# Optimization experiments

Hardware: AMD Instinct MI355X
Metric: run time of the kernel (lower is better)

The kernel has to match this reference:

```python
import jax, jax.numpy as jnp
import numpy as np
from jax import lax

B, S, DM = 4, 4096, 1024
H, P, R = 16, 32, 8
D = DM // H  # head_dim = 64
K_SEL = 4


def setup_inputs() -> dict:
    key = jax.random.key(0)
    ks = jax.random.split(key, 6)
    x = jax.random.normal(ks[0], (B, S, DM), dtype=jnp.float32)
    K_state = jax.random.normal(ks[1], (H, P, R, D), dtype=jnp.float32) / np.sqrt(D)
    V_state = jax.random.normal(ks[2], (H, P, R, D), dtype=jnp.float32) / np.sqrt(D)
    W_router = jax.random.normal(ks[3], (H, D, P), dtype=jnp.float32) / np.sqrt(D)
    W_out = jax.random.normal(ks[4], (DM, DM), dtype=jnp.float32) / np.sqrt(DM)
    b_out = jnp.zeros((DM,), dtype=jnp.float32)
    return {"x": x, "K_state": K_state, "V_state": V_state,
            "W_router": W_router, "W_out": W_out, "b_out": b_out, "k": K_SEL}


def reference(x, K_state, V_state, W_router, W_out, b_out, k):
    b, s, dm = x.shape
    h, p, r, d = K_state.shape
    xh = x.reshape(b, s, h, d)  # per-head token features

    # Router: top-k partition selection per token per head.
    logits = jnp.einsum('bshd,hdp->bshp', xh, W_router)
    topv = lax.top_k(logits, k)[0]            # [b,s,h,k]
    thresh = topv[..., -1:]                   # k-th largest logit
    neg_inf = jnp.array(-jnp.inf, dtype=logits.dtype)
    gates = jax.nn.softmax(jnp.where(logits >= thresh, logits, neg_inf), axis=-1)  # [b,s,h,p], zero off top-k

    # Attention over state rows within each partition (masked-dense == sparse gather math).
    scale = jnp.asarray(1.0 / np.sqrt(d), dtype=x.dtype)
    scores = jnp.einsum('bshd,hprd->bshpr', xh, K_state) * scale
    attn = jax.nn.softmax(scores, axis=-1)    # softmax over rows r within a partition

    # Gate-weighted combine of per-partition attention outputs, fused to avoid [b,s,h,p,d].
    w = attn * gates[..., None]               # [b,s,h,p,r]
    heads = jnp.einsum('bshpr,hprd->bshd', w, V_state)

    out = heads.reshape(b, s, dm) @ W_out + b_out
    return out
```

## Files before the change

kernel.cpp:

```cpp
#include <hip/hip_runtime.h>
#include <hip/hip_bf16.h>

#define BB 4
#define SS 4096
#define DM 1024
#define HH 16
#define PP 32
#define RR 8
#define DD 64
#define NTOK (BB*SS)
#define MM NTOK
#define NN DM
#define KK DM

typedef __attribute__((ext_vector_type(8))) short short8;
typedef __attribute__((ext_vector_type(4))) float floatx4;

static __device__ inline short f2bf(float f) {
    union { __hip_bfloat16 b; short s; } u; u.b = __float2bfloat16(f); return u.s;
}
static __device__ inline short8 pack8(float4 lo, float4 hi) {
    short8 r;
    r[0] = f2bf(lo.x); r[1] = f2bf(lo.y); r[2] = f2bf(lo.z); r[3] = f2bf(lo.w);
    r[4] = f2bf(hi.x); r[5] = f2bf(hi.y); r[6] = f2bf(hi.z); r[7] = f2bf(hi.w);
    return r;
}

static __device__ inline unsigned bfr(float f) {
    unsigned u = __float_as_uint(f);
    return u + 0x7fffu + ((u >> 16) & 1u);
}
static __device__ inline int pk2(float a, float b) {
    return __builtin_amdgcn_perm(bfr(b), bfr(a), 0x07060302);
}
static __device__ inline short8 pk8(float4 lo, float4 hi) {
    union { short8 s; int i[4]; } r;
    r.i[0] = pk2(lo.x, lo.y); r.i[1] = pk2(lo.z, lo.w);
    r.i[2] = pk2(hi.x, hi.y); r.i[3] = pk2(hi.z, hi.w);
    return r.s;
}

__global__ __launch_bounds__(256) void pre_fused(const float* __restrict__ x,
                                                 const float* __restrict__ Wr,
                                                 const int* __restrict__ kp,
                                                 const float* __restrict__ Wo,
                                                 const float* __restrict__ Kst,
                                                 const float* __restrict__ Vst,
                                                 float* __restrict__ gates_g,
                                                 __hip_bfloat16* __restrict__ wsw,
                                                 __hip_bfloat16* __restrict__ kfrag,
                                                 __hip_bfloat16* __restrict__ vfrag,
                                                 __hip_bfloat16* __restrict__ xbf) {
    const int bx = blockIdx.x;

    if (bx >= 4096) {
        if (bx < 4608) {
            int tid = (bx - 4096) * 256 + threadIdx.x;
            int l = tid & 63;
            int kblk = (tid >> 6) & 31;
            int ntile = tid >> 11;
            int col = ntile * 16 + (l & 15);
            int krow = kblk * 32 + (l >> 4) * 8;
#pragma unroll
            for (int j = 0; j < 8; ++j)
                wsw[(size_t)tid * 8 + j] = __float2bfloat16(Wo[(size_t)(krow + j) * NN + col]);
        } else if (bx < 4864) {
            int tid = (bx - 4608) * 256 + threadIdx.x;
            int arr = tid >> 15;
            int idx = tid & 32767;
            int h = idx >> 11, blk = (idx >> 6) & 31, fl = idx & 63;
            int fm = fl & 15, fk = fl >> 4;
            short8 val;
            short* dst;
            if (arr == 0) {
                int mt = blk >> 1, kb = blk & 1;
                int pr = mt * 16 + fm, d0 = kb * 32 + fk * 8;
                const float* src = Kst + ((size_t)h * 256 + pr) * 64 + d0;
                float4 lo = *(const float4*)src, hi = *(const float4*)(src + 4);
                val = pack8(lo, hi);
                dst = (short*)kfrag + (size_t)idx * 8;
            } else {
                int mt = blk >> 3, kb = blk & 7;
                int d = mt * 16 + fm, pr0 = kb * 32 + fk * 8;
                const float* src = Vst + ((size_t)h * 256 + pr0) * 64 + d;
#pragma unroll
                for (int j = 0; j < 8; ++j) val[j] = f2bf(src[j * 64]);
                dst = (short*)vfrag + (size_t)idx * 8;
            }
            *(short8*)dst = val;
        } else {
            int xid = bx - 4864;
            int tile = xid & 255, h = xid >> 8;
            int lane = threadIdx.x & 63, w = threadIdx.x >> 6;
            int l15 = lane & 15, l4 = lane >> 4;
            const float* srcb = x + (size_t)(tile * 64 + w * 16 + l15) * DM + h * 64 + l4 * 8;
            short* dstb = (short*)xbf + ((size_t)((h * 256 + tile) * 8 + w * 2) * 512) + lane * 8;
#pragma unroll
            for (int kb = 0; kb < 2; ++kb) {
                float4 lo = *(const float4*)(srcb + kb * 32);
                float4 hi = *(const float4*)(srcb + kb * 32 + 4);
                *(short8*)(dstb + kb * 512) = pk8(lo, hi);
            }
        }
        return;
    }

    __shared__ __align__(16) char smem[26624];
    float (*xs)[68] = (float (*)[68])smem;
    float (*Lg)[36] = (float (*)[36])(smem + 17408);

    const int lane = threadIdx.x & 63;
    const int w = threadIdx.x >> 6;
    const int l15 = lane & 15, l4 = lane >> 4;
    const int tile = bx & 255;
    const int h = bx >> 8;
    const int t0 = tile * 64;

    {
        int row = threadIdx.x >> 2, q = threadIdx.x & 3;
        const float4* src = (const float4*)(x + (size_t)(t0 + row) * DM + h * 64 + q * 16);
        float4 v0 = src[0], v1 = src[1], v2 = src[2], v3 = src[3];
        float4* dst = (float4*)&xs[row][q * 16];
        dst[0] = v0; dst[1] = v1; dst[2] = v2; dst[3] = v3;
    }

    const int p = lane & 31, dh = lane >> 5;
    float wreg[32];
    {
        const float* wrp = Wr + (size_t)h * (DD * PP) + dh * 32 * PP + p;
#pragma unroll
        for (int dd = 0; dd < 32; ++dd) wreg[dd] = wrp[dd * PP];
    }
    const int kkv = kp[0];

    __syncthreads();

    for (int it = 0; it < 16; it += 2) {
        const int ta = w * 16 + it;
        const int tb = ta + 1;
        float la = 0.f, lb = 0.f;
#pragma unroll
        for (int j = 0; j < 8; ++j) {
            float4 qa = *(const float4*)&xs[ta][dh * 32 + 4 * j];
            float4 qb = *(const float4*)&xs[tb][dh * 32 + 4 * j];
            la += qa.x * wreg[4 * j];     lb += qb.x * wreg[4 * j];
            la += qa.y * wreg[4 * j + 1]; lb += qb.y * wreg[4 * j + 1];
            la += qa.z * wreg[4 * j + 2]; lb += qb.z * wreg[4 * j + 2];
            la += qa.w * wreg[4 * j + 3]; lb += qb.w * wreg[4 * j + 3];
        }
        la += __shfl_xor(la, 32);
        lb += __shfl_xor(lb, 32);
        if (lane < 32) {
            Lg[ta][lane] = la;
            Lg[tb][lane] = lb;
        }
    }
    __syncthreads();

    float thresh = 0.f, a1 = 0.f;
    if (lane < 16) {
        int t = w * 16 + lane;
        float lgr[32];
        const float4* lrow = (const float4*)&Lg[t][0];
#pragma unroll
        for (int c = 0; c < 8; ++c) {
            float4 q4 = lrow[c];
            lgr[4 * c] = q4.x; lgr[4 * c + 1] = q4.y; lgr[4 * c + 2] = q4.z; lgr[4 * c + 3] = q4.w;
        }
        float aa = -INFINITY, b2 = -INFINITY, c3 = -INFINITY, d4 = -INFINITY;
#pragma unroll
        for (int pp = 0; pp < 32; ++pp) {
            float v = lgr[pp];
            float na = fmaxf(aa, v); v = fminf(aa, v); aa = na;
            float nb = fmaxf(b2, v); v = fminf(b2, v); b2 = nb;
            float nc = fmaxf(c3, v); v = fminf(c3, v); c3 = nc;
            d4 = fmaxf(d4, v);
        }
        thresh = (kkv >= 4) ? d4 : (kkv == 3 ? c3 : (kkv == 2 ? b2 : aa));
        a1 = aa;
    }
    thresh = __shfl(thresh, l15);
    a1     = __shfl(a1, l15);

    {
        const int t = w * 16 + l15;
        const int p8 = l4 * 8;
        const float4* lrow = (const float4*)&Lg[t][p8];
        float4 qa = lrow[0], qb = lrow[1];
        float e0 = (qa.x >= thresh) ? __expf(qa.x - a1) : 0.f;
        float e1 = (qa.y >= thresh) ? __expf(qa.y - a1) : 0.f;
        float e2 = (qa.z >= thresh) ? __expf(qa.z - a1) : 0.f;
        float e3 = (qa.w >= thresh) ? __expf(qa.w - a1) : 0.f;
        float e4 = (qb.x >= thresh) ? __expf(qb.x - a1) : 0.f;
        float e5 = (qb.y >= thresh) ? __expf(qb.y - a1) : 0.f;
        float e6 = (qb.z >= thresh) ? __expf(qb.z - a1) : 0.f;
        float e7 = (qb.w >= thresh) ? __expf(qb.w - a1) : 0.f;
        float part = ((e0 + e1) + (e2 + e3)) + ((e4 + e5) + (e6 + e7));
        part += __shfl_xor(part, 16);
        part += __shfl_xor(part, 32);
        float inv = 1.f / part;
        float* gb = gates_g + ((size_t)(h * 256 + tile) * 32) * 64 + t;
        gb[(p8 + 0) * 64] = e0 * inv;
        gb[(p8 + 1) * 64] = e1 * inv;
        gb[(p8 + 2) * 64] = e2 * inv;
        gb[(p8 + 3) * 64] = e3 * inv;
        gb[(p8 + 4) * 64] = e4 * inv;
        gb[(p8 + 5) * 64] = e5 * inv;
        gb[(p8 + 6) * 64] = e6 * inv;
        gb[(p8 + 7) * 64] = e7 * inv;
    }
}

__global__ __launch_bounds__(256, 3) void attn_mm(const __hip_bfloat16* __restrict__ xbf,
                                                  const __hip_bfloat16* __restrict__ kfrag,
                                                  const __hip_bfloat16* __restrict__ vfrag,
                                                  const float* __restrict__ gates_g,
                                                  __hip_bfloat16* __restrict__ hb) {
    __shared__ __align__(16) short wf[16384];

    const int lane = threadIdx.x & 63;
    const int w = threadIdx.x >> 6;
    const int l15 = lane & 15, l4 = lane >> 4;
    const int t0 = blockIdx.x * 64;
    const int h = blockIdx.y;

    const float* gb = gates_g + ((size_t)(h * 256 + blockIdx.x) * 32) * 64;
    float gv[4][4];
#pragma unroll
    for (int mi = 0; mi < 4; ++mi) {
        const int pidx = (w * 4 + mi) * 2 + (l4 >> 1);
#pragma unroll
        for (int nt = 0; nt < 4; ++nt)
            gv[mi][nt] = gb[pidx * 64 + nt * 16 + l15];
    }

    const short* xbase = (const short*)xbf + ((size_t)(h * 256 + blockIdx.x) * 8) * 512 + lane * 8;
    short8 xb[4][2];
#pragma unroll
    for (int nt = 0; nt < 4; ++nt)
#pragma unroll
        for (int kb = 0; kb < 2; ++kb)
            xb[nt][kb] = *(const short8*)(xbase + (nt * 2 + kb) * 512);
    short8 ka[4][2];
#pragma unroll
    for (int mi = 0; mi < 4; ++mi)
#pragma unroll
        for (int kb = 0; kb < 2; ++kb)
            ka[mi][kb] = *(const short8*)((const short*)kfrag +
                          ((size_t)(h * 32 + (w * 4 + mi) * 2 + kb) * 512 + lane * 8));

    floatx4 acc[4][4] = {};
#pragma unroll
    for (int kb = 0; kb < 2; ++kb)
#pragma unroll
        for (int mi = 0; mi < 4; ++mi)
#pragma unroll
            for (int nt = 0; nt < 4; ++nt)
                acc[mi][nt] = __builtin_amdgcn_mfma_f32_16x16x32_bf16(ka[mi][kb], xb[nt][kb], acc[mi][nt], 0, 0, 0);

#pragma unroll
    for (int mi = 0; mi < 4; ++mi) {
        const int mt = w * 4 + mi;
#pragma unroll
        for (int nt = 0; nt < 4; ++nt) {
            float g = gv[mi][nt];
            float s0 = acc[mi][nt][0] * 0.125f;
            float s1 = acc[mi][nt][1] * 0.125f;
            float s2 = acc[mi][nt][2] * 0.125f;
            float s3 = acc[mi][nt][3] * 0.125f;
            float mx = fmaxf(fmaxf(s0, s1), fmaxf(s2, s3));
            mx = fmaxf(mx, __shfl_xor(mx, 16));
            float e0 = __expf(s0 - mx), e1 = __expf(s1 - mx);
            float e2 = __expf(s2 - mx), e3 = __expf(s3 - mx);
            float loc = (e0 + e1) + (e2 + e3);
            float se = loc + __shfl_xor(loc, 16);
            float ws = g / se;
            int2 pk;
            pk.x = pk2(e0 * ws, e1 * ws);
            pk.y = pk2(e2 * ws, e3 * ws);
            int off = (((mt & 1) * 2 + (l4 >> 1)) * 16 + l15) * 8 + (l4 & 1) * 4;
            *(int2*)&wf[(nt * 8 + (mt >> 1)) * 512 + off] = pk;
        }
    }
    __syncthreads();

    floatx4 h4[4] = {};
#pragma unroll
    for (int kb = 0; kb < 8; ++kb) {
        short8 va = *(const short8*)((const short*)vfrag +
                      ((size_t)(h * 32 + w * 8 + kb) * 512 + lane * 8));
#pragma unroll
        for (int nt = 0; nt < 4; ++nt) {
            short8 wb = *(const short8*)&wf[(nt * 8 + kb) * 512 + lane * 8];
            h4[nt] = __builtin_amdgcn_mfma_f32_16x16x32_bf16(va, wb, h4[nt], 0, 0, 0);
        }
    }
#pragma unroll
    for (int nt = 0; nt < 4; ++nt) {
        int t = t0 + nt * 16 + l15;
        int2 pk;
        pk.x = pk2(h4[nt][0], h4[nt][1]);
        pk.y = pk2(h4[nt][2], h4[nt][3]);
        *(int2*)((short*)hb + (size_t)t * DM + h * 64 + w * 16 + l4 * 4) = pk;
    }
}

__global__ __launch_bounds__(256) void gemm_v6(const __hip_bfloat16* __restrict__ Abf,
                                               const __hip_bfloat16* __restrict__ Bsw,
                                               const float* __restrict__ bias,
                                               float* __restrict__ C) {
    __shared__ __align__(16) short As[2][8192];
    const int lane = threadIdx.x & 63;
    const int wave = threadIdx.x >> 6;
    const int wm = wave >> 1, wn = wave & 1;

    const int wg  = blockIdx.y * 8 + blockIdx.x;
    const int xcd = wg & 7;
    const int loc = wg >> 3;
    const int bm0 = (xcd * 16 + (loc >> 3)) * 128;
    const int bn0 = (loc & 7) * 128;

    const int l15 = lane & 15, l4 = lane >> 4;

    const short* Ap = (const short*)Abf;
    const short* Bp = (const short*)Bsw;

    int crow[4], ck8[4];
#pragma unroll
    for (int j = 0; j < 4; ++j) {
        int c = (wave * 4 + j) * 64 + lane;
        int row = c >> 3;
        crow[j] = row;
        ck8[j] = ((c & 7) ^ (row & 7)) * 8;
    }

    int boff[4];
#pragma unroll
    for (int nt = 0; nt < 4; ++nt)
        boff[nt] = (((bn0 >> 4) + wn * 4 + nt) * 32) * 512 + lane * 8;

    const int axor = l15 & 7;
    int arow[4];
#pragma unroll
    for (int mt = 0; mt < 4; ++mt)
        arow[mt] = (wm * 64 + mt * 16 + l15) * 64;
    const int ak0 = (l4 ^ axor) * 8;
    const int ak1 = ((4 + l4) ^ axor) * 8;

    floatx4 acc[4][4] = {};

#pragma unroll
    for (int j = 0; j < 4; ++j)
        __builtin_amdgcn_global_load_lds(
            (const __attribute__((address_space(1))) unsigned int*)
                (Ap + (size_t)(bm0 + crow[j]) * KK + ck8[j]),
            (__attribute__((address_space(3))) unsigned int*)&As[0][(wave * 4 + j) * 512],
            16, 0, 0);
    short8 bA[4];
#pragma unroll
    for (int nt = 0; nt < 4; ++nt)
        bA[nt] = *(const short8*)(Bp + boff[nt]);
    __syncthreads();

    for (int step = 0; step < 16; ++step) {
        const int cur = step & 1;
        const int nxt = cur ^ 1;

        short8 bB[4];
#pragma unroll
        for (int nt = 0; nt < 4; ++nt)
            bB[nt] = *(const short8*)(Bp + boff[nt] + (size_t)(2 * step + 1) * 512);

        short8 bN[4];
        if (step < 15) {
#pragma unroll
            for (int nt = 0; nt < 4; ++nt)
                bN[nt] = *(const short8*)(Bp + boff[nt] + (size_t)(2 * step + 2) * 512);
#pragma unroll
            for (int j = 0; j < 4; ++j)
                __builtin_amdgcn_global_load_lds(
                    (const __attribute__((address_space(1))) unsigned int*)
                        (Ap + (size_t)(bm0 + crow[j]) * KK + (step + 1) * 64 + ck8[j]),
                    (__attribute__((address_space(3))) unsigned int*)&As[nxt][(wave * 4 + j) * 512],
                    16, 0, 0);
        }

        short8 a0[4];
#pragma unroll
        for (int mt = 0; mt < 4; ++mt)
            a0[mt] = *(const short8*)&As[cur][arow[mt] + ak0];
#pragma unroll
        for (int mt = 0; mt < 4; ++mt)
#pragma unroll
            for (int nt = 0; nt < 4; ++nt)
                acc[mt][nt] = __builtin_amdgcn_mfma_f32_16x16x32_bf16(a0[mt], bA[nt], acc[mt][nt], 0, 0, 0);

        short8 a1[4];
#pragma unroll
        for (int mt = 0; mt < 4; ++mt)
            a1[mt] = *(const short8*)&As[cur][arow[mt] + ak1];
#pragma unroll
        for (int mt = 0; mt < 4; ++mt)
#pragma unroll
            for (int nt = 0; nt < 4; ++nt)
                acc[mt][nt] = __builtin_amdgcn_mfma_f32_16x16x32_bf16(a1[mt], bB[nt], acc[mt][nt], 0, 0, 0);

        if (step < 15) {
#pragma unroll
            for (int nt = 0; nt < 4; ++nt)
                bA[nt] = bN[nt];
        }
        __syncthreads();
    }

#pragma unroll
    for (int nt = 0; nt < 4; ++nt) {
        const int col = bn0 + wn * 64 + nt * 16 + l15;
        const float bv = bias[col];
#pragma unroll
        for (int mt = 0; mt < 4; ++mt) {
            const int row0 = bm0 + wm * 64 + mt * 16 + l4 * 4;
#pragma unroll
            for (int i = 0; i < 4; ++i)
                C[(size_t)(row0 + i) * NN + col] = acc[mt][nt][i] + bv;
        }
    }
}

extern "C" void kernel_launch(void* const* d_in, const int* in_sizes, int n_in,
                              void* d_out, int out_size, void* d_ws, size_t ws_size,
                              hipStream_t stream) {
    const float* x   = (const float*)d_in[0];
    const float* Kst = (const float*)d_in[1];
    const float* Vst = (const float*)d_in[2];
    const float* Wr  = (const float*)d_in[3];
    const float* Wo  = (const float*)d_in[4];
    const float* bo  = (const float*)d_in[5];
    const int*   kp  = (const int*)d_in[6];
    float* out = (float*)d_out;

    __hip_bfloat16* hb    = (__hip_bfloat16*)d_ws;
    __hip_bfloat16* wsw   = hb + (size_t)MM * KK;
    __hip_bfloat16* kfrag = wsw + (size_t)KK * NN;
    __hip_bfloat16* vfrag = kfrag + 16 * 32 * 512;
    float* gates_g = (float*)(vfrag + 16 * 32 * 512);
    __hip_bfloat16* xbf = (__hip_bfloat16*)d_out;

    pre_fused<<<dim3(8960), 256, 0, stream>>>(x, Wr, kp, Wo, Kst, Vst,
                                              gates_g, wsw, kfrag, vfrag, xbf);
    attn_mm<<<dim3(NTOK / 64, HH), 256, 0, stream>>>(xbf, kfrag, vfrag, gates_g, hb);
    gemm_v6<<<dim3(NN / 128, MM / 128), 256, 0, stream>>>(hb, wsw, bo, out);
}
```

Before: 230.1 us.

## Triple-buffer A tile in LDS with partial vmcnt waits in output GEMM

Replaces the double-buffered LDS A-tile pipeline in the output projection GEMM with a three-stage ring. Loads are now issued two K-steps ahead, and the full __syncthreads is swapped for a raw s_barrier preceded by s_waitcnt vmcnt(4), so the newest prefetch can stay in flight across the barrier. The aim is to hide global-to-LDS latency better. In exchange it uses 50% more shared memory, which may reduce occupancy. It also relies on how the B register loads and the LDS loads are ordered in the vmcnt queue.

```diff
diff --git a/kernel.cpp b/kernel.cpp
--- a/kernel.cpp
+++ b/kernel.cpp
@@ -305,11 +305,11 @@
     }
 }
 
-__global__ __launch_bounds__(256) void gemm_v6(const __hip_bfloat16* __restrict__ Abf,
+__global__ __launch_bounds__(256) void gemm_v7(const __hip_bfloat16* __restrict__ Abf,
                                                const __hip_bfloat16* __restrict__ Bsw,
                                                const float* __restrict__ bias,
                                                float* __restrict__ C) {
-    __shared__ __align__(16) short As[2][8192];
+    __shared__ __align__(16) short As[3][8192];
     const int lane = threadIdx.x & 63;
     const int wave = threadIdx.x >> 6;
     const int wm = wave >> 1, wn = wave & 1;
@@ -349,46 +349,52 @@
 
     floatx4 acc[4][4] = {};
 
-#pragma unroll
-    for (int j = 0; j < 4; ++j)
-        __builtin_amdgcn_global_load_lds(
-            (const __attribute__((address_space(1))) unsigned int*)
-                (Ap + (size_t)(bm0 + crow[j]) * KK + ck8[j]),
-            (__attribute__((address_space(3))) unsigned int*)&As[0][(wave * 4 + j) * 512],
-            16, 0, 0);
     short8 bA[4];
 #pragma unroll
     for (int nt = 0; nt < 4; ++nt)
         bA[nt] = *(const short8*)(Bp + boff[nt]);
-    __syncthreads();
+#pragma unroll
+    for (int s = 0; s < 2; ++s)
+#pragma unroll
+        for (int j = 0; j < 4; ++j)
+            __builtin_amdgcn_global_load_lds(
+                (const __attribute__((address_space(1))) unsigned int*)
+                    (Ap + (size_t)(bm0 + crow[j]) * KK + s * 64 + ck8[j]),
+                (__attribute__((address_space(3))) unsigned int*)&As[s][(wave * 4 + j) * 512],
+                16, 0, 0);
+    asm volatile("s_waitcnt vmcnt(4)" ::: "memory");
+    __builtin_amdgcn_s_barrier();
+    __builtin_amdgcn_sched_barrier(0);
 
     for (int step = 0; step < 16; ++step) {
-        const int cur = step & 1;
-        const int nxt = cur ^ 1;
+        const short* curb = As[step % 3];
 
         short8 bB[4];
 #pragma unroll
         for (int nt = 0; nt < 4; ++nt)
             bB[nt] = *(const short8*)(Bp + boff[nt] + (size_t)(2 * step + 1) * 512);
-
         short8 bN[4];
         if (step < 15) {
 #pragma unroll
             for (int nt = 0; nt < 4; ++nt)
                 bN[nt] = *(const short8*)(Bp + boff[nt] + (size_t)(2 * step + 2) * 512);
+        }
+        __builtin_amdgcn_sched_barrier(0);
+        if (step < 14) {
+            short* nb = As[(step + 2) % 3];
 #pragma unroll
             for (int j = 0; j < 4; ++j)
                 __builtin_amdgcn_global_load_lds(
                     (const __attribute__((address_space(1))) unsigned int*)
-                        (Ap + (size_t)(bm0 + crow[j]) * KK + (step + 1) * 64 + ck8[j]),
-                    (__attribute__((address_space(3))) unsigned int*)&As[nxt][(wave * 4 + j) * 512],
+                        (Ap + (size_t)(bm0 + crow[j]) * KK + (step + 2) * 64 + ck8[j]),
+                    (__attribute__((address_space(3))) unsigned int*)&nb[(wave * 4 + j) * 512],
                     16, 0, 0);
         }
 
         short8 a0[4];
 #pragma unroll
         for (int mt = 0; mt < 4; ++mt)
-            a0[mt] = *(const short8*)&As[cur][arow[mt] + ak0];
+            a0[mt] = *(const short8*)&curb[arow[mt] + ak0];
 #pragma unroll
         for (int mt = 0; mt < 4; ++mt)
 #pragma unroll
@@ -398,7 +404,7 @@
         short8 a1[4];
 #pragma unroll
         for (int mt = 0; mt < 4; ++mt)
-            a1[mt] = *(const short8*)&As[cur][arow[mt] + ak1];
+            a1[mt] = *(const short8*)&curb[arow[mt] + ak1];
 #pragma unroll
         for (int mt = 0; mt < 4; ++mt)
 #pragma unroll
@@ -410,7 +416,9 @@
             for (int nt = 0; nt < 4; ++nt)
                 bA[nt] = bN[nt];
         }
-        __syncthreads();
+        asm volatile("s_waitcnt vmcnt(4)" ::: "memory");
+        __builtin_amdgcn_s_barrier();
+        __builtin_amdgcn_sched_barrier(0);
     }
 
 #pragma unroll
@@ -449,5 +457,5 @@
     pre_fused<<<dim3(8960), 256, 0, stream>>>(x, Wr, kp, Wo, Kst, Vst,
                                               gates_g, wsw, kfrag, vfrag, xbf);
     attn_mm<<<dim3(NTOK / 64, HH), 256, 0, stream>>>(xbf, kfrag, vfrag, gates_g, hb);
-    gemm_v6<<<dim3(NN / 128, MM / 128), 256, 0, stream>>>(hb, wsw, bo, out);
-}
+    gemm_v7<<<dim3(NN / 128, MM / 128), 256, 0, stream>>>(hb, wsw, bo, out);
+}
```

New measurement: 228.1 us. Within noise of the previous version (-0.9%).
